# Kernel tuning notes

Hardware: AMD Instinct MI355X
Metric: run time of the kernel (lower is better)

## Reference

```python
import jax, jax.numpy as jnp
import numpy as np

HEAD = 8

def setup_inputs() -> dict:
    key = jax.random.key(0)
    ks = jax.random.split(key, 11)
    B, C, W, H = 16, 512, 32, 32
    d, N = C // HEAD, W * H
    return {
        "x": jax.random.normal(ks[0], (B, C, W, H), jnp.float32),
        "Wq": jax.random.normal(ks[1], (C, C), jnp.float32) * 0.02,
        "bq": jax.random.normal(ks[2], (C,), jnp.float32) * 0.02,
        "Wk": jax.random.normal(ks[3], (C, C), jnp.float32) * 0.02,
        "bk": jax.random.normal(ks[4], (C,), jnp.float32) * 0.02,
        "Wv": jax.random.normal(ks[5], (C, C), jnp.float32) * 0.02,
        "bv": jax.random.normal(ks[6], (C,), jnp.float32) * 0.02,
        "rel_h": jax.random.normal(ks[7], (1, HEAD, d, 1, H), jnp.float32),
        "rel_w": jax.random.normal(ks[8], (1, HEAD, d, W, 1), jnp.float32),
        "reg_qk": jax.random.normal(ks[9], (1, N, N), jnp.float32),
        "reg_v": jax.random.normal(ks[10], (1, d, N), jnp.float32),
    }

def reference(x, Wq, bq, Wk, bk, Wv, bv, rel_h, rel_w, reg_qk, reg_v):
    B, C, W, H = x.shape
    head = HEAD
    d = C // head
    N = W * H
    def conv1x1(inp, Wt, b):  # 1x1 conv == per-pixel linear
        return jnp.einsum('bchw,oc->bohw', inp, Wt) + b[None, :, None, None]
    q = conv1x1(x, Wq, bq).reshape(B, head, d, N)
    k = conv1x1(x, Wk, bk).reshape(B, head, d, N)
    v = conv1x1(x, Wv, bv).reshape(B, head, d, N)
    # content-content: q^T k -> [B, head, N, N]
    cc = jnp.einsum('bhdn,bhdm->bhnm', q, k)
    # content-position: (rel_h + rel_w) broadcast to [1, head, d, W, H] -> [head, N, d]
    pos = (rel_h + rel_w).reshape(head, d, N)
    cp = jnp.einsum('hdn,bhdm->bhnm', pos, q)
    energy = cc + cp  # [B, head, N, N]
    n_reg = reg_qk.shape[0]
    energy = jnp.concatenate(
        [energy, jnp.broadcast_to(reg_qk[None], (B, n_reg, N, N))], axis=1)
    v_all = jnp.concatenate(
        [v, jnp.broadcast_to(reg_v[None], (B, n_reg, d, N))], axis=1)
    attn = jax.nn.softmax(energy, axis=-1)  # [B, head+n_reg, N, N]
    # v @ attn^T
    out = jnp.einsum('bgdn,bgmn->bgdm', v_all, attn)
    out = out[:, :head].reshape(B, C, W, H)
    return out + x
```

## Files before the change

kernel.cpp:

```cpp
#include <hip/hip_runtime.h>

#define BB   16
#define HEADS 8
#define DH   64
#define NSP  1024
#define CCH  512

typedef unsigned int   u32;
typedef unsigned short u16;
typedef __attribute__((ext_vector_type(8))) short  short8;
typedef __attribute__((ext_vector_type(4))) float  floatx4;

#if defined(__has_builtin)
#if __has_builtin(__builtin_amdgcn_exp2f)
#define EXP2F(x) __builtin_amdgcn_exp2f(x)
#else
#define EXP2F(x) exp2f(x)
#endif
#else
#define EXP2F(x) exp2f(x)
#endif

__device__ __forceinline__ u16 f2b(float f) {
  u32 x = __float_as_uint(f);
  x = x + 0x7fffu + ((x >> 16) & 1u);
  return (u16)(x >> 16);
}

__device__ __forceinline__ u32 pkbf(float lo, float hi) {
  return __builtin_amdgcn_perm(__float_as_uint(hi) + 0x8000u,
                               __float_as_uint(lo) + 0x8000u, 0x07060302u);
}

__device__ __forceinline__ void gload_lds16(const u16* g, u16* l) {
  __builtin_amdgcn_global_load_lds((const __attribute__((address_space(1))) u32*)g,
                                   (__attribute__((address_space(3))) u32*)l, 16, 0, 0);
}

__global__ __launch_bounds__(256) void prep_all(const float* __restrict__ x,
                                                const float* __restrict__ Wq,
                                                const float* __restrict__ Wk,
                                                const float* __restrict__ Wv,
                                                const float* __restrict__ rel_h,
                                                const float* __restrict__ rel_w,
                                                u16* __restrict__ wbf,
                                                u16* __restrict__ pos,
                                                u16* __restrict__ xt) {
  __shared__ float ld[64][68];
  int bid = blockIdx.x;
  int t = threadIdx.x;
  if (bid < 768) {
    int idx = bid * 256 + t;
    int which = idx >> 16;
    int r4 = (idx & 65535) * 4;
    const float* src = which == 0 ? Wq : which == 1 ? Wk : Wv;
    float4 v = *(const float4*)&src[r4];
    ushort4 s;
    s.x = f2b(v.x); s.y = f2b(v.y); s.z = f2b(v.z); s.w = f2b(v.w);
    *(ushort4*)&wbf[(which << 18) + r4] = s;
  } else if (bid < 2816) {
    int idx = (bid - 768) * 256 + t;
    int dd = idx & 63;
    int n  = (idx >> 6) & 1023;
    int h  = idx >> 16;
    int ww = n >> 5, hh = n & 31;
    float v = rel_h[(h * 64 + dd) * 32 + hh] + rel_w[(h * 64 + dd) * 32 + ww];
    pos[idx] = f2b(v);
  } else {
    int bid2 = bid - 2816;
    int ntile = bid2 & 15, ctile = (bid2 >> 4) & 7, b = bid2 >> 7;
    const float* xb = x + (((size_t)b * CCH + ctile * 64) << 10) + ntile * 64;
#pragma unroll
    for (int p = 0; p < 4; ++p) {
      int c = p * 16 + (t >> 4), n4 = (t & 15) * 4;
      float4 v = *(const float4*)&xb[((size_t)c << 10) + n4];
      ld[c][n4 + 0] = v.x; ld[c][n4 + 1] = v.y; ld[c][n4 + 2] = v.z; ld[c][n4 + 3] = v.w;
    }
    __syncthreads();
    u16* xo = xt + (((size_t)b << 10) + ntile * 64) * CCH + ctile * 64;
#pragma unroll
    for (int p = 0; p < 2; ++p) {
      int id = p * 256 + t;
      int n = id >> 3, c8 = (id & 7) * 8;
      ushort4 s0, s1;
      s0.x = f2b(ld[c8 + 0][n]); s0.y = f2b(ld[c8 + 1][n]);
      s0.z = f2b(ld[c8 + 2][n]); s0.w = f2b(ld[c8 + 3][n]);
      s1.x = f2b(ld[c8 + 4][n]); s1.y = f2b(ld[c8 + 5][n]);
      s1.z = f2b(ld[c8 + 6][n]); s1.w = f2b(ld[c8 + 7][n]);
      *(ushort4*)&xo[(size_t)n * CCH + c8] = s0;
      *(ushort4*)&xo[(size_t)n * CCH + c8 + 4] = s1;
    }
  }
}

__global__ __launch_bounds__(256, 2) void qkv_mfma(const u16* __restrict__ wbf,
                                                   const u16* __restrict__ xt,
                                                   const float* __restrict__ bq,
                                                   const float* __restrict__ bk,
                                                   const float* __restrict__ bv,
                                                   u16* __restrict__ qw,
                                                   u16* __restrict__ kw,
                                                   u16* __restrict__ vtw) {
  int ntile = blockIdx.x, otile = blockIdx.y;
  int b = blockIdx.z & 15, which = blockIdx.z >> 4;
  int o0 = otile * 128, n0 = ntile * 128;

  __shared__ __align__(16) u16 smem[2 * 16384];

  int t = threadIdx.x;
  int w = t >> 6, lane = t & 63;
  int l15 = lane & 15, quad = lane >> 4;
  int wrM = (w >> 1) * 64, wrN = (w & 1) * 64;

  const u16* Ag = wbf + ((size_t)which << 18) + (size_t)o0 * CCH;
  const u16* Bg = xt + (((size_t)b << 10) + n0) * CCH;

  floatx4 acc[4][4];
#pragma unroll
  for (int i = 0; i < 4; ++i)
#pragma unroll
    for (int j = 0; j < 4; ++j) acc[i][j] = (floatx4){0.f, 0.f, 0.f, 0.f};

  int srow = lane >> 3;
  int scc = ((lane & 7) ^ srow) << 3;

  auto stage = [&](int k0, int buf) {
    u16* At = smem + buf * 16384;
    u16* Bt = At + 8192;
#pragma unroll
    for (int p = 0; p < 4; ++p) {
      int r0 = (w * 4 + p) * 8;
      int row = r0 + srow;
      gload_lds16(Ag + (size_t)row * CCH + k0 + scc, &At[r0 * 64]);
      gload_lds16(Bg + (size_t)row * CCH + k0 + scc, &Bt[r0 * 64]);
    }
  };

  stage(0, 0);

  for (int ki = 0; ki < 8; ++ki) {
    __syncthreads();
    if (ki < 7) stage((ki + 1) * 64, (ki + 1) & 1);

    u16* At = smem + (ki & 1) * 16384;
    u16* Bt = At + 8192;
    const u16* aSrc = which == 2 ? Bt : At;
    const u16* bSrc = which == 2 ? At : Bt;

#pragma unroll
    for (int ks = 0; ks < 2; ++ks) {
      short8 af[4], bf4[4];
#pragma unroll
      for (int s = 0; s < 4; ++s) {
        int ra = wrM + s * 16 + l15;
        int rb = wrN + s * 16 + l15;
        af[s]  = *(const short8*)&aSrc[ra * 64 + (((ks * 4 + quad) ^ (ra & 7)) << 3)];
        bf4[s] = *(const short8*)&bSrc[rb * 64 + (((ks * 4 + quad) ^ (rb & 7)) << 3)];
      }
#pragma unroll
      for (int i = 0; i < 4; ++i)
#pragma unroll
        for (int j = 0; j < 4; ++j)
          acc[i][j] = __builtin_amdgcn_mfma_f32_16x16x32_bf16(af[i], bf4[j], acc[i][j], 0, 0, 0);
    }
  }

  if (which == 2) {
#pragma unroll
    for (int i = 0; i < 4; ++i) {
      int n = n0 + wrM + i * 16 + quad * 4;
      int nt = n >> 6, nn = n & 63;
#pragma unroll
      for (int j = 0; j < 4; ++j) {
        int o = o0 + wrN + j * 16 + l15;
        int h = o >> 6, dd = o & 63;
        float bias = bv[o];
        uint2 s;
        s.x = pkbf(acc[i][j][0] + bias, acc[i][j][1] + bias);
        s.y = pkbf(acc[i][j][2] + bias, acc[i][j][3] + bias);
        *(uint2*)&vtw[(((size_t)(b * HEADS + h) * 16 + nt) * 64 + dd) * 64 + nn] = s;
      }
    }
  } else {
    const float* bias = which == 0 ? bq : bk;
    u16* dst = which == 0 ? qw : kw;
#pragma unroll
    for (int i = 0; i < 4; ++i) {
      int o = o0 + wrM + i * 16 + quad * 4;
      int h = o >> 6, dd = o & 63;
      float b0 = bias[o], b1 = bias[o + 1], b2 = bias[o + 2], b3 = bias[o + 3];
      size_t hb = (size_t)(b * HEADS + h) * NSP;
#pragma unroll
      for (int j = 0; j < 4; ++j) {
        int n = n0 + wrN + j * 16 + l15;
        uint2 s;
        s.x = pkbf(acc[i][j][0] + b0, acc[i][j][1] + b1);
        s.y = pkbf(acc[i][j][2] + b2, acc[i][j][3] + b3);
        *(uint2*)&dst[(hb + n) * 64 + dd] = s;
      }
    }
  }
}

__global__ __launch_bounds__(256, 2) void attn_mfma(const u16* __restrict__ qw,
                                                    const u16* __restrict__ kw,
                                                    const u16* __restrict__ vtw,
                                                    const u16* __restrict__ pos,
                                                    const float* __restrict__ x,
                                                    float* __restrict__ out) {
  int bh = blockIdx.x, mtile = blockIdx.y;
  int b = bh >> 3, h = bh & 7;
  __shared__ __align__(16) u16 smem_u16[34816];
  u16* pt = smem_u16 + 24576;

  int t = threadIdx.x;
  int w = t >> 6, lane = t & 63;
  int l15 = lane & 15, quad = lane >> 4;
  size_t bhs = (size_t)bh;

  short8 qa[4][2], pa[4][2];
  {
    const short* qg = (const short*)qw + (bhs * NSP + mtile * 256 + w * 64) * 64;
    const short* pg = (const short*)pos + ((size_t)h * NSP + mtile * 256 + w * 64) * 64;
#pragma unroll
    for (int msub = 0; msub < 4; ++msub)
#pragma unroll
      for (int ks = 0; ks < 2; ++ks) {
        int off = (msub * 16 + l15) * 64 + ks * 32 + quad * 8;
        qa[msub][ks] = *(const short8*)(qg + off);
        pa[msub][ks] = *(const short8*)(pg + off);
      }
  }

  floatx4 oacc[4][4];
  float lsum[4] = {0.f, 0.f, 0.f, 0.f};
#pragma unroll
  for (int i = 0; i < 4; ++i)
#pragma unroll
    for (int j = 0; j < 4; ++j) oacc[i][j] = (floatx4){0.f, 0.f, 0.f, 0.f};

  const u16* kg  = kw + bhs * NSP * 64;
  const u16* qgn = qw + bhs * NSP * 64;
  const u16* vg  = vtw + bhs * 16 * 4096;
  u16* ptw = pt + w * 2560;
  int srow = lane >> 3, sc = lane & 7;

  int rs = l15 & 7;
  int c0 = (quad ^ rs) << 3;
  int c1 = ((4 + quad) ^ rs) << 3;

  auto stage = [&](int nt, int buf) {
    u16* kt = smem_u16 + buf * 12288;
    u16* qt = kt + 4096;
    u16* vt = qt + 4096;
#pragma unroll
    for (int p = 0; p < 2; ++p) {
      int r0 = w * 16 + p * 8;
      int row = r0 + srow;
      int swz = ((sc ^ (row & 7)) << 3);
      gload_lds16(kg + (nt * 64 + row) * 64 + swz, &kt[r0 * 64]);
      gload_lds16(qgn + (nt * 64 + row) * 64 + swz, &qt[r0 * 64]);
      gload_lds16(vg + (size_t)nt * 4096 + row * 64 + swz, &vt[r0 * 64]);
    }
  };

  stage(0, 0);

  for (int nt = 0; nt < 16; ++nt) {
    __syncthreads();
    if (nt < 15) stage(nt + 1, (nt + 1) & 1);

    u16* kt = smem_u16 + (nt & 1) * 12288;
    u16* qt = kt + 4096;
    u16* vt = qt + 4096;

#pragma unroll
    for (int half = 0; half < 2; ++half) {
#pragma unroll
      for (int nblk2 = 0; nblk2 < 2; ++nblk2) {
        int nblk = half * 2 + nblk2;
        int rb = (nblk * 16 + l15) * 64;
        short8 kb0 = *(short8*)&kt[rb + c0];
        short8 kb1 = *(short8*)&kt[rb + c1];
        short8 qb0 = *(short8*)&qt[rb + c0];
        short8 qb1 = *(short8*)&qt[rb + c1];
        floatx4 sc4[4];
#pragma unroll
        for (int msub = 0; msub < 4; ++msub) {
          floatx4 c = (floatx4){0.f, 0.f, 0.f, 0.f};
          c = __builtin_amdgcn_mfma_f32_16x16x32_bf16(kb0, qa[msub][0], c, 0, 0, 0);
          c = __builtin_amdgcn_mfma_f32_16x16x32_bf16(kb1, qa[msub][1], c, 0, 0, 0);
          c = __builtin_amdgcn_mfma_f32_16x16x32_bf16(qb0, pa[msub][0], c, 0, 0, 0);
          c = __builtin_amdgcn_mfma_f32_16x16x32_bf16(qb1, pa[msub][1], c, 0, 0, 0);
          sc4[msub] = c;
        }
#pragma unroll
        for (int msub = 0; msub < 4; ++msub) {
          float p0 = EXP2F(fmaf(sc4[msub][0], 1.44269504f, -11.5415603f));
          float p1 = EXP2F(fmaf(sc4[msub][1], 1.44269504f, -11.5415603f));
          float p2 = EXP2F(fmaf(sc4[msub][2], 1.44269504f, -11.5415603f));
          float p3 = EXP2F(fmaf(sc4[msub][3], 1.44269504f, -11.5415603f));
          lsum[msub] += (p0 + p1) + (p2 + p3);
          uint2 pk;
          pk.x = pkbf(p0, p1);
          pk.y = pkbf(p2, p3);
          *(uint2*)&ptw[(msub * 16 + l15) * 40 + nblk2 * 16 + quad * 4] = pk;
        }
      }
      short8 pB[4];
#pragma unroll
      for (int msub = 0; msub < 4; ++msub)
        pB[msub] = *(short8*)&ptw[(msub * 16 + l15) * 40 + quad * 8];
#pragma unroll
      for (int dd = 0; dd < 4; ++dd) {
        int row = dd * 16 + l15;
        short8 vb = *(short8*)&vt[row * 64 + (((half * 4 + quad) ^ (row & 7)) << 3)];
#pragma unroll
        for (int msub = 0; msub < 4; ++msub)
          oacc[msub][dd] = __builtin_amdgcn_mfma_f32_16x16x32_bf16(vb, pB[msub], oacc[msub][dd], 0, 0, 0);
      }
    }
  }

  float rinv[4];
#pragma unroll
  for (int msub = 0; msub < 4; ++msub) {
    float l = lsum[msub];
    l += __shfl_xor(l, 16);
    l += __shfl_xor(l, 32);
    rinv[msub] = 1.0f / l;
  }

  __syncthreads();
  float* ot = (float*)smem_u16 + w * 2304;
  int l8 = lane & 7, lr = lane >> 3;
#pragma unroll
  for (int mh = 0; mh < 2; ++mh) {
#pragma unroll
    for (int ms2 = 0; ms2 < 2; ++ms2) {
      int msub = mh * 2 + ms2;
#pragma unroll
      for (int dd = 0; dd < 4; ++dd)
#pragma unroll
        for (int r = 0; r < 4; ++r)
          ot[(dd * 16 + quad * 4 + r) * 36 + ms2 * 16 + l15] = oacc[msub][dd][r] * rinv[msub];
    }
#pragma unroll
    for (int pass = 0; pass < 8; ++pass) {
      int dd = pass * 8 + lr;
      float4 o4 = *(float4*)&ot[dd * 36 + l8 * 4];
      size_t off = (((size_t)b * CCH + h * DH + dd) << 10) + mtile * 256 + w * 64 + mh * 32 + l8 * 4;
      float4 xv = *(const float4*)&x[off];
      o4.x += xv.x; o4.y += xv.y; o4.z += xv.z; o4.w += xv.w;
      *(float4*)&out[off] = o4;
    }
  }
}

extern "C" void kernel_launch(void* const* d_in, const int* in_sizes, int n_in,
                              void* d_out, int out_size, void* d_ws, size_t ws_size,
                              hipStream_t stream) {
  const float* x     = (const float*)d_in[0];
  const float* Wq    = (const float*)d_in[1];
  const float* bq    = (const float*)d_in[2];
  const float* Wk    = (const float*)d_in[3];
  const float* bk    = (const float*)d_in[4];
  const float* Wv    = (const float*)d_in[5];
  const float* bv    = (const float*)d_in[6];
  const float* rel_h = (const float*)d_in[7];
  const float* rel_w = (const float*)d_in[8];
  float* out = (float*)d_out;

  char* ws = (char*)d_ws;
  u16* qw   = (u16*)(ws);
  u16* kw   = (u16*)(ws + ((size_t)16 << 20));
  u16* vtw  = (u16*)(ws + ((size_t)32 << 20));
  u16* pos  = (u16*)(ws + ((size_t)48 << 20));
  u16* wbf  = (u16*)(ws + ((size_t)49 << 20));
  u16* xt   = (u16*)d_out;

  hipLaunchKernelGGL(prep_all, dim3(4864), dim3(256), 0, stream,
                     x, Wq, Wk, Wv, rel_h, rel_w, wbf, pos, xt);
  hipLaunchKernelGGL(qkv_mfma, dim3(8, 4, 48), dim3(256), 0, stream,
                     wbf, xt, bq, bk, bv, qw, kw, vtw);
  hipLaunchKernelGGL(attn_mfma, dim3(128, 4), dim3(256), 0, stream,
                     qw, kw, vtw, pos, x, out);
}
```

Before: 215.7 us.

## Fuse Q/K/V projections into one kernel sharing the x tile, stage epilogue via LDS

```diff
diff --git a/kernel.cpp b/kernel.cpp
--- a/kernel.cpp
+++ b/kernel.cpp
@@ -93,48 +93,55 @@
   }
 }
 
-__global__ __launch_bounds__(256, 2) void qkv_mfma(const u16* __restrict__ wbf,
-                                                   const u16* __restrict__ xt,
-                                                   const float* __restrict__ bq,
-                                                   const float* __restrict__ bk,
-                                                   const float* __restrict__ bv,
-                                                   u16* __restrict__ qw,
-                                                   u16* __restrict__ kw,
-                                                   u16* __restrict__ vtw) {
-  int ntile = blockIdx.x, otile = blockIdx.y;
-  int b = blockIdx.z & 15, which = blockIdx.z >> 4;
-  int o0 = otile * 128, n0 = ntile * 128;
-
-  __shared__ __align__(16) u16 smem[2 * 16384];
+__global__ __launch_bounds__(256, 2) void qkv_fused(const u16* __restrict__ wbf,
+                                                    const u16* __restrict__ xt,
+                                                    const float* __restrict__ bq,
+                                                    const float* __restrict__ bk,
+                                                    const float* __restrict__ bv,
+                                                    u16* __restrict__ qw,
+                                                    u16* __restrict__ kw,
+                                                    u16* __restrict__ vtw) {
+  int ntile = blockIdx.x, otile = blockIdx.y, b = blockIdx.z;
+  int o0 = otile * 64, n0 = ntile * 128;
+
+  __shared__ __align__(16) u16 smem[2 * 20480];
 
   int t = threadIdx.x;
   int w = t >> 6, lane = t & 63;
   int l15 = lane & 15, quad = lane >> 4;
-  int wrM = (w >> 1) * 64, wrN = (w & 1) * 64;
-
-  const u16* Ag = wbf + ((size_t)which << 18) + (size_t)o0 * CCH;
-  const u16* Bg = xt + (((size_t)b << 10) + n0) * CCH;
-
-  floatx4 acc[4][4];
-#pragma unroll
-  for (int i = 0; i < 4; ++i)
-#pragma unroll
-    for (int j = 0; j < 4; ++j) acc[i][j] = (floatx4){0.f, 0.f, 0.f, 0.f};
-
-  int srow = lane >> 3;
-  int scc = ((lane & 7) ^ srow) << 3;
+  int srow = lane >> 3, sc = lane & 7;
+  int scc = (sc ^ srow) << 3;
+
+  floatx4 aq[8], ak[8], av[8];
+#pragma unroll
+  for (int i = 0; i < 8; ++i) {
+    aq[i] = (floatx4){0.f, 0.f, 0.f, 0.f};
+    ak[i] = (floatx4){0.f, 0.f, 0.f, 0.f};
+    av[i] = (floatx4){0.f, 0.f, 0.f, 0.f};
+  }
 
   auto stage = [&](int k0, int buf) {
-    u16* At = smem + buf * 16384;
-    u16* Bt = At + 8192;
-#pragma unroll
-    for (int p = 0; p < 4; ++p) {
-      int r0 = (w * 4 + p) * 8;
-      int row = r0 + srow;
-      gload_lds16(Ag + (size_t)row * CCH + k0 + scc, &At[r0 * 64]);
-      gload_lds16(Bg + (size_t)row * CCH + k0 + scc, &Bt[r0 * 64]);
+    u16* base = smem + buf * 20480;
+#pragma unroll
+    for (int p = 0; p < 10; ++p) {
+      int g0 = w * 80 + p * 8;
+      if (g0 < 192) {
+        int which = g0 >> 6;
+        int r0 = g0 & 63;
+        gload_lds16(wbf + ((size_t)which << 18) + (size_t)(o0 + r0 + srow) * CCH + k0 + scc,
+                    base + which * 4096 + r0 * 64);
+      } else {
+        int r0 = g0 - 192;
+        gload_lds16(xt + (size_t)(b * 1024 + n0 + r0 + srow) * CCH + k0 + scc,
+                    base + 12288 + r0 * 64);
+      }
     }
   };
+
+  int rs = l15 & 7;
+  int c0 = (quad ^ rs) << 3;
+  int c1 = ((4 + quad) ^ rs) << 3;
+  int wrow = (w * 16 + l15) * 64;
 
   stage(0, 0);
 
@@ -142,62 +149,69 @@
     __syncthreads();
     if (ki < 7) stage((ki + 1) * 64, (ki + 1) & 1);
 
-    u16* At = smem + (ki & 1) * 16384;
-    u16* Bt = At + 8192;
-    const u16* aSrc = which == 2 ? Bt : At;
-    const u16* bSrc = which == 2 ? At : Bt;
-
+    u16* base = smem + (ki & 1) * 20480;
+    u16* Xb = base + 12288;
 #pragma unroll
     for (int ks = 0; ks < 2; ++ks) {
-      short8 af[4], bf4[4];
-#pragma unroll
-      for (int s = 0; s < 4; ++s) {
-        int ra = wrM + s * 16 + l15;
-        int rb = wrN + s * 16 + l15;
-        af[s]  = *(const short8*)&aSrc[ra * 64 + (((ks * 4 + quad) ^ (ra & 7)) << 3)];
-        bf4[s] = *(const short8*)&bSrc[rb * 64 + (((ks * 4 + quad) ^ (rb & 7)) << 3)];
+      int cc = ks ? c1 : c0;
+      short8 fq = *(short8*)&base[wrow + cc];
+      short8 fk = *(short8*)&base[4096 + wrow + cc];
+      short8 fv = *(short8*)&base[8192 + wrow + cc];
+#pragma unroll
+      for (int ns = 0; ns < 8; ++ns) {
+        short8 fx = *(short8*)&Xb[(ns * 16 + l15) * 64 + cc];
+        aq[ns] = __builtin_amdgcn_mfma_f32_16x16x32_bf16(fq, fx, aq[ns], 0, 0, 0);
+        ak[ns] = __builtin_amdgcn_mfma_f32_16x16x32_bf16(fk, fx, ak[ns], 0, 0, 0);
+        av[ns] = __builtin_amdgcn_mfma_f32_16x16x32_bf16(fx, fv, av[ns], 0, 0, 0);
       }
-#pragma unroll
-      for (int i = 0; i < 4; ++i)
-#pragma unroll
-        for (int j = 0; j < 4; ++j)
-          acc[i][j] = __builtin_amdgcn_mfma_f32_16x16x32_bf16(af[i], bf4[j], acc[i][j], 0, 0, 0);
-    }
-  }
-
-  if (which == 2) {
+    }
+  }
+
+  __syncthreads();
+  u16* epQ = smem;
+  u16* epK = smem + 9216;
+  u16* epV = smem + 18432;
+  {
+    int ob = o0 + w * 16 + quad * 4;
+    float q0 = bq[ob], q1 = bq[ob + 1], q2 = bq[ob + 2], q3 = bq[ob + 3];
+    float k0b = bk[ob], k1b = bk[ob + 1], k2b = bk[ob + 2], k3b = bk[ob + 3];
+    float vb = bv[o0 + w * 16 + l15];
+#pragma unroll
+    for (int ns = 0; ns < 8; ++ns) {
+      int n = ns * 16 + l15;
+      uint2 pk;
+      pk.x = pkbf(aq[ns][0] + q0, aq[ns][1] + q1);
+      pk.y = pkbf(aq[ns][2] + q2, aq[ns][3] + q3);
+      *(uint2*)&epQ[n * 72 + w * 16 + quad * 4] = pk;
+      pk.x = pkbf(ak[ns][0] + k0b, ak[ns][1] + k1b);
+      pk.y = pkbf(ak[ns][2] + k2b, ak[ns][3] + k3b);
+      *(uint2*)&epK[n * 72 + w * 16 + quad * 4] = pk;
+      pk.x = pkbf(av[ns][0] + vb, av[ns][1] + vb);
+      pk.y = pkbf(av[ns][2] + vb, av[ns][3] + vb);
+      *(uint2*)&epV[(w * 16 + l15) * 136 + ns * 16 + quad * 4] = pk;
+    }
+  }
+  __syncthreads();
+  int h = otile;
+  {
+    int row = t >> 1, half = t & 1;
+    size_t gb = ((size_t)(b * HEADS + h) * NSP + n0 + row) * 64 + half * 32;
+#pragma unroll
+    for (int i = 0; i < 4; ++i)
+      *(uint4*)&qw[gb + i * 8] = *(uint4*)&epQ[row * 72 + half * 32 + i * 8];
+#pragma unroll
+    for (int i = 0; i < 4; ++i)
+      *(uint4*)&kw[gb + i * 8] = *(uint4*)&epK[row * 72 + half * 32 + i * 8];
+  }
+  {
+    int row = t >> 2, q4 = t & 3;
 #pragma unroll
     for (int i = 0; i < 4; ++i) {
-      int n = n0 + wrM + i * 16 + quad * 4;
-      int nt = n >> 6, nn = n & 63;
-#pragma unroll
-      for (int j = 0; j < 4; ++j) {
-        int o = o0 + wrN + j * 16 + l15;
-        int h = o >> 6, dd = o & 63;
-        float bias = bv[o];
-        uint2 s;
-        s.x = pkbf(acc[i][j][0] + bias, acc[i][j][1] + bias);
-        s.y = pkbf(acc[i][j][2] + bias, acc[i][j][3] + bias);
-        *(uint2*)&vtw[(((size_t)(b * HEADS + h) * 16 + nt) * 64 + dd) * 64 + nn] = s;
-      }
-    }
-  } else {
-    const float* bias = which == 0 ? bq : bk;
-    u16* dst = which == 0 ? qw : kw;
-#pragma unroll
-    for (int i = 0; i < 4; ++i) {
-      int o = o0 + wrM + i * 16 + quad * 4;
-      int h = o >> 6, dd = o & 63;
-      float b0 = bias[o], b1 = bias[o + 1], b2 = bias[o + 2], b3 = bias[o + 3];
-      size_t hb = (size_t)(b * HEADS + h) * NSP;
-#pragma unroll
-      for (int j = 0; j < 4; ++j) {
-        int n = n0 + wrN + j * 16 + l15;
-        uint2 s;
-        s.x = pkbf(acc[i][j][0] + b0, acc[i][j][1] + b1);
-        s.y = pkbf(acc[i][j][2] + b2, acc[i][j][3] + b3);
-        *(uint2*)&dst[(hb + n) * 64 + dd] = s;
-      }
+      int nl = q4 * 32 + i * 8;
+      int n = n0 + nl;
+      int ntl = n >> 6, nn = n & 63;
+      *(uint4*)&vtw[(((size_t)(b * HEADS + h) * 16 + ntl) * 64 + row) * 64 + nn]
+          = *(uint4*)&epV[row * 136 + nl];
     }
   }
 }
@@ -381,7 +395,7 @@
 
   hipLaunchKernelGGL(prep_all, dim3(4864), dim3(256), 0, stream,
                      x, Wq, Wk, Wv, rel_h, rel_w, wbf, pos, xt);
-  hipLaunchKernelGGL(qkv_mfma, dim3(8, 4, 48), dim3(256), 0, stream,
+  hipLaunchKernelGGL(qkv_fused, dim3(8, 8, 16), dim3(256), 0, stream,
                      wbf, xt, bq, bk, bv, qw, kw, vtw);
   hipLaunchKernelGGL(attn_mfma, dim3(128, 4), dim3(256), 0, stream,
                      qw, kw, vtw, pos, x, out);
```

Result: faster. 210.2 us (-2.5%).
